# Kernel tuning notes

Measured on AMD Instinct MI355X. Metric: run time of the kernel, lower is better.

## Reference

```python
import jax, jax.numpy as jnp
import numpy as np

B, S, D, H = 2, 2048, 1024, 16
DH = D // H
EPS = 1e-5
NEG = -1e9


def _layer_norm(x, g, b):
    m = jnp.mean(x, axis=-1, keepdims=True)
    v = jnp.mean(jnp.square(x - m), axis=-1, keepdims=True)
    return (x - m) * jax.lax.rsqrt(v + EPS) * g + b


def setup_inputs() -> dict:
    key = jax.random.key(0)
    ks = jax.random.split(key, 10)
    std = 0.02
    inp = {
        "x": jax.random.normal(ks[0], (B, S, D), dtype=jnp.float32),
        "src_mask": jax.random.randint(ks[1], (B, S), 0, 2) > 0,
        # projection weights stored as (in, out) so y = x @ w + b
        "wq": jax.random.normal(ks[2], (D, D), dtype=jnp.float32) * std,
        "bq": jnp.zeros((D,), jnp.float32),
        "wk": jax.random.normal(ks[3], (D, D), dtype=jnp.float32) * std,
        "bk": jnp.zeros((D,), jnp.float32),
        "wv": jax.random.normal(ks[4], (D, D), dtype=jnp.float32) * std,
        "bv": jnp.zeros((D,), jnp.float32),
        "wo": jax.random.normal(ks[5], (D, D), dtype=jnp.float32) * std,
        "bo": jnp.zeros((D,), jnp.float32),
        "ln1_g": jnp.ones((D,), jnp.float32),
        "ln1_b": jnp.zeros((D,), jnp.float32),
        "w1": jax.random.normal(ks[6], (D, 2 * D), dtype=jnp.float32) * std,
        "b1": jnp.zeros((2 * D,), jnp.float32),
        "w2": jax.random.normal(ks[7], (2 * D, D), dtype=jnp.float32) * std,
        "b2": jnp.zeros((D,), jnp.float32),
        "ln2_g": jnp.ones((D,), jnp.float32),
        "ln2_b": jnp.zeros((D,), jnp.float32),
    }
    return inp


def reference(x, src_mask, wq, bq, wk, bk, wv, bv, wo, bo,
              ln1_g, ln1_b, w1, b1, w2, b2, ln2_g, ln2_b):
    b, s, d = x.shape
    # Q/K/V projections, split into heads: [B, S, H, DH]
    q = (x @ wq + bq).reshape(b, s, H, DH)
    k = (x @ wk + bk).reshape(b, s, H, DH)
    v = (x @ wv + bv).reshape(b, s, H, DH)
    # scaled scores [B, H, Sq, Sk] (matches torch's split/cat over heads)
    scores = jnp.einsum('bqhd,bkhd->bhqk', q, k) / jnp.sqrt(jnp.float32(DH))
    # additive key mask: -1e9 where src_mask is False
    scores = scores + jnp.where(src_mask, 0.0, NEG)[:, None, None, :]
    A = jax.nn.softmax(scores, axis=-1)
    attn = jnp.einsum('bhqk,bkhd->bqhd', A, v).reshape(b, s, d)
    attn_out = attn @ wo + bo + x
    h = _layer_norm(attn_out, ln1_g, ln1_b)
    ffn = jax.nn.relu(h @ w1 + b1) @ w2 + b2
    return _layer_norm(ffn + h, ln2_g, ln2_b)
```

## Files before the change

kernel.cpp:

```cpp
#include <hip/hip_runtime.h>
#include <math.h>

#define BB  2
#define SS  2048
#define DD  1024
#define HH  16
#define DHH 64
#define MM  (BB * SS)

typedef float f32x4 __attribute__((ext_vector_type(4)));
typedef short s16x8 __attribute__((ext_vector_type(8)));

__device__ __forceinline__ unsigned short f2b(float f) {
    union { float f; unsigned u; } v; v.f = f;
    unsigned r = v.u + 0x7fffu + ((v.u >> 16) & 1u);
    return (unsigned short)(r >> 16);
}
__device__ __forceinline__ float b2f(unsigned short u) {
    union { unsigned u; float f; } v; v.u = ((unsigned)u) << 16;
    return v.f;
}
__device__ __forceinline__ unsigned cvtpk(float lo, float hi) {
    unsigned r;
    asm("v_cvt_pk_bf16_f32 %0, %1, %2" : "=v"(r) : "v"(lo), "v"(hi));
    return r;
}

typedef __attribute__((address_space(1))) void gv_t;
typedef __attribute__((address_space(3))) void lv_t;
__device__ __forceinline__ void gld16(const void* g, void* l) {
    __builtin_amdgcn_global_load_lds((gv_t*)(void*)g, (lv_t*)l, 16, 0, 0);
}

__device__ __forceinline__ int sidx(int row, int col) {
    return row * 64 + (col ^ (((row + (row >> 3)) & 7) << 3));
}

template <int RELU, int RES, int OUTF, int VS>
__global__ __launch_bounds__(256)
void mgemm(const unsigned short* __restrict__ A, const unsigned short* __restrict__ B,
           const float* __restrict__ bias, const void* __restrict__ res,
           void* __restrict__ out, unsigned short* __restrict__ vt,
           int M, int N, int K, int outN)
{
    __shared__ short As[128 * 64];
    __shared__ short Bs[128 * 64];

    const int tid  = threadIdx.x;
    const int wave = tid >> 6, lane = tid & 63;
    const int bm = blockIdx.y * 128, bn = blockIdx.x * 128;
    const int srow = tid >> 3;
    const int scol = (tid & 7) * 8;
    const int wr = wave >> 1, wc = wave & 1;
    const int fr = lane & 15;
    const int fk = (lane >> 4) * 8;

    f32x4 acc[4][4];
#pragma unroll
    for (int i = 0; i < 4; ++i)
#pragma unroll
        for (int j = 0; j < 4; ++j) acc[i][j] = (f32x4){0.f, 0.f, 0.f, 0.f};

    for (int k0 = 0; k0 < K; k0 += 64) {
#pragma unroll
        for (int it = 0; it < 4; ++it) {
            gld16(&A[(size_t)(bm + it * 32 + srow) * K + k0 + scol],
                  &As[it * 2048 + wave * 512]);
            gld16(&B[(size_t)(bn + it * 32 + srow) * K + k0 + scol],
                  &Bs[it * 2048 + wave * 512]);
        }
        __syncthreads();

#pragma unroll
        for (int kk = 0; kk < 2; ++kk) {
            s16x8 af[4], bf[4];
#pragma unroll
            for (int i = 0; i < 4; ++i)
                af[i] = *(const s16x8*)&As[(wr * 64 + i * 16 + fr) * 64 + kk * 32 + fk];
#pragma unroll
            for (int j = 0; j < 4; ++j)
                bf[j] = *(const s16x8*)&Bs[(wc * 64 + j * 16 + fr) * 64 + kk * 32 + fk];
#pragma unroll
            for (int i = 0; i < 4; ++i)
#pragma unroll
                for (int j = 0; j < 4; ++j)
                    acc[i][j] = __builtin_amdgcn_mfma_f32_16x16x32_bf16(
                        af[i], bf[j], acc[i][j], 0, 0, 0);
        }
        __syncthreads();
    }

    const int r0 = bm + wr * 64 + (lane >> 4) * 4;
    const int c0 = bn + wc * 64 + (lane & 15);
    const float* resf          = (const float*)res;
    const unsigned short* resh = (const unsigned short*)res;
    float* outf          = (float*)out;
    unsigned short* outh = (unsigned short*)out;

    if (VS == 1 && bn >= 2048) {
#pragma unroll
        for (int i = 0; i < 4; ++i)
#pragma unroll
            for (int j = 0; j < 4; ++j) {
                const int col = c0 + j * 16;
                const int hh = (col >> 6) & 15, dh = col & 63;
                const float bcol = bias[col];
#pragma unroll
                for (int r = 0; r < 4; ++r) {
                    const int row = r0 + i * 16 + r;
                    const int bb = row >> 11, s = row & 2047;
                    vt[(size_t)(((bb * 16 + hh) * 64) + dh) * 2048 + s] =
                        f2b(acc[i][j][r] + bcol);
                }
            }
        return;
    }

#pragma unroll
    for (int i = 0; i < 4; ++i)
#pragma unroll
        for (int j = 0; j < 4; ++j) {
            const int col = c0 + j * 16;
            const float bcol = bias[col];
#pragma unroll
            for (int r = 0; r < 4; ++r) {
                const int row = r0 + i * 16 + r;
                float v = acc[i][j][r] + bcol;
                if (RES == 1) v += resf[(size_t)row * outN + col];
                if (RES == 2) v += b2f(resh[(size_t)row * outN + col]);
                if (RELU)     v = fmaxf(v, 0.f);
                if (OUTF) outf[(size_t)row * outN + col] = v;
                else      outh[(size_t)row * outN + col] = f2b(v);
            }
        }
}

__global__ __launch_bounds__(256)
void prep(const float* __restrict__ x,
          const float* __restrict__ wq, const float* __restrict__ wk,
          const float* __restrict__ wv, const float* __restrict__ wo,
          const float* __restrict__ w1, const float* __restrict__ w2,
          const float* __restrict__ bq, const float* __restrict__ bk,
          const float* __restrict__ bv,
          unsigned short* __restrict__ xb, unsigned short* __restrict__ wqkvT,
          unsigned short* __restrict__ woT, unsigned short* __restrict__ w1T,
          unsigned short* __restrict__ w2T, float* __restrict__ bqkv)
{
    __shared__ float T[64][65];
    const int tid = threadIdx.x;
    int bid = blockIdx.x;

    if (bid < 4096) {
        const int i = bid * 256 + tid;
        const float4 v = ((const float4*)x)[i];
        ushort4 o4;
        o4.x = f2b(v.x); o4.y = f2b(v.y); o4.z = f2b(v.z); o4.w = f2b(v.w);
        ((ushort4*)xb)[i] = o4;
        return;
    }
    bid -= 4096;

    if (bid >= 2048) {
        const int i = (bid - 2048) * 256 + tid;
        if (i < 1024) bqkv[i] = bq[i];
        else if (i < 2048) bqkv[i] = bk[i - 1024];
        else if (i < 3072) bqkv[i] = bv[i - 2048];
        return;
    }

    const float* src; unsigned short* dst; int K, N, nbx, sub;
    if (bid < 256)       { src = wq; dst = wqkvT;               K = 1024; N = 1024; nbx = 16; sub = bid; }
    else if (bid < 512)  { src = wk; dst = wqkvT + 1024 * 1024; K = 1024; N = 1024; nbx = 16; sub = bid - 256; }
    else if (bid < 768)  { src = wv; dst = wqkvT + 2048 * 1024; K = 1024; N = 1024; nbx = 16; sub = bid - 512; }
    else if (bid < 1024) { src = wo; dst = woT;                 K = 1024; N = 1024; nbx = 16; sub = bid - 768; }
    else if (bid < 1536) { src = w1; dst = w1T;                 K = 1024; N = 2048; nbx = 32; sub = bid - 1024; }
    else                 { src = w2; dst = w2T;                 K = 2048; N = 1024; nbx = 16; sub = bid - 1536; }

    const int n0 = (sub % nbx) * 64, k0 = (sub / nbx) * 64;
    const int c = tid & 63, rb = tid >> 6;
#pragma unroll
    for (int it = 0; it < 16; ++it) {
        const int r = it * 4 + rb;
        T[r][c] = src[(size_t)(k0 + r) * N + n0 + c];
    }
    __syncthreads();
#pragma unroll
    for (int it = 0; it < 16; ++it) {
        const int r = it * 4 + rb;
        dst[(size_t)(n0 + r) * K + k0 + c] = f2b(T[c][r]);
    }
}

__global__ __launch_bounds__(512)
void attn_mfma(const unsigned short* __restrict__ qk,
               const unsigned short* __restrict__ vt,
               const int* __restrict__ mask, unsigned short* __restrict__ o)
{
    const int b = blockIdx.z, h = blockIdx.y, q0 = blockIdx.x * 128;
    __shared__ unsigned short QP[8192];
    __shared__ unsigned short Ks[4096];
    __shared__ unsigned short Vs[4096];
    __shared__ float maskf[64];
    const int tid = threadIdx.x, wave = tid >> 6, lane = tid & 63;
    const int grp = lane >> 4, l16 = lane & 15;

    const size_t qkbase = (size_t)(b * SS) * 2048 + h * DHH;
    const size_t vbase  = (size_t)((b * HH + h) * 64) * 2048;
    const float SC = 0.18033688f;
    const float MNEG = -1.442695e9f;

#pragma unroll
    for (int it = 0; it < 2; ++it) {
        const int slot = it * 512 + tid;
        const int row = slot >> 3, dhb = slot & 7;
        const int src = (dhb ^ ((row + (row >> 3)) & 7)) * 8;
        gld16(&qk[qkbase + (size_t)(q0 + row) * 2048 + src],
              &QP[it * 4096 + wave * 512]);
    }
    const int krow = tid >> 3, kdhb = tid & 7;
    const int ksrc = (kdhb ^ ((krow + (krow >> 3)) & 7)) * 8;
    __syncthreads();
    const int prow = wave * 16 + l16;
    const s16x8 aq0 = *(const s16x8*)&QP[sidx(prow, grp * 8)];
    const s16x8 aq1 = *(const s16x8*)&QP[sidx(prow, 32 + grp * 8)];

    const s16x8 ones = {(short)0x3F80, (short)0x3F80, (short)0x3F80, (short)0x3F80,
                        (short)0x3F80, (short)0x3F80, (short)0x3F80, (short)0x3F80};

    f32x4 accO[4];
#pragma unroll
    for (int j = 0; j < 4; ++j) accO[j] = (f32x4){0.f, 0.f, 0.f, 0.f};
    f32x4 accS = (f32x4){0.f, 0.f, 0.f, 0.f};
    float mrow = -1e30f;

    for (int kt = 0; kt < SS / 64; ++kt) {
        const int kv0 = kt * 64;
        __syncthreads();
        gld16(&qk[qkbase + (size_t)(kv0 + krow) * 2048 + 1024 + ksrc], &Ks[wave * 512]);
        gld16(&vt[vbase + (size_t)krow * 2048 + kv0 + ksrc],           &Vs[wave * 512]);
        if (tid < 64) maskf[tid] = mask[b * SS + kv0 + tid] ? 0.f : MNEG;
        __syncthreads();

        f32x4 sv[4];
        __builtin_amdgcn_s_setprio(1);
#pragma unroll
        for (int j = 0; j < 4; ++j) {
            const s16x8 bk0 = *(const s16x8*)&Ks[sidx(j * 16 + l16, grp * 8)];
            const s16x8 bk1 = *(const s16x8*)&Ks[sidx(j * 16 + l16, 32 + grp * 8)];
            f32x4 z = (f32x4){0.f, 0.f, 0.f, 0.f};
            z = __builtin_amdgcn_mfma_f32_16x16x32_bf16(bk0, aq0, z, 0, 0, 0);
            z = __builtin_amdgcn_mfma_f32_16x16x32_bf16(bk1, aq1, z, 0, 0, 0);
            sv[j] = z;
        }
        __builtin_amdgcn_s_setprio(0);
#pragma unroll
        for (int j = 0; j < 4; ++j) {
            const float4 mv = *(const float4*)&maskf[j * 16 + grp * 4];
            sv[j][0] = sv[j][0] * SC + mv.x;
            sv[j][1] = sv[j][1] * SC + mv.y;
            sv[j][2] = sv[j][2] * SC + mv.z;
            sv[j][3] = sv[j][3] * SC + mv.w;
        }

        float mx = -1e30f;
#pragma unroll
        for (int j = 0; j < 4; ++j)
#pragma unroll
            for (int r = 0; r < 4; ++r) mx = fmaxf(mx, sv[j][r]);
        mx = fmaxf(mx, __shfl_xor(mx, 16));
        mx = fmaxf(mx, __shfl_xor(mx, 32));

        if (!__all(mx <= mrow + 8.f)) {
            const float mnew = fmaxf(mrow, mx);
            const float corrq = __builtin_amdgcn_exp2f(mrow - mnew);
            mrow = mnew;
            float cr[4];
#pragma unroll
            for (int r = 0; r < 4; ++r) cr[r] = __shfl(corrq, grp * 4 + r);
#pragma unroll
            for (int r = 0; r < 4; ++r) {
                accS[r] *= cr[r];
#pragma unroll
                for (int j = 0; j < 4; ++j) accO[j][r] *= cr[r];
            }
        }

#pragma unroll
        for (int j = 0; j < 4; ++j) {
            const float p0 = __builtin_amdgcn_exp2f(sv[j][0] - mrow);
            const float p1 = __builtin_amdgcn_exp2f(sv[j][1] - mrow);
            const float p2 = __builtin_amdgcn_exp2f(sv[j][2] - mrow);
            const float p3 = __builtin_amdgcn_exp2f(sv[j][3] - mrow);
            *(unsigned*)&QP[sidx(prow, j * 16 + grp * 4)]     = cvtpk(p0, p1);
            *(unsigned*)&QP[sidx(prow, j * 16 + grp * 4 + 2)] = cvtpk(p2, p3);
        }

        const s16x8 pa0 = *(const s16x8*)&QP[sidx(prow, grp * 8)];
        const s16x8 pa1 = *(const s16x8*)&QP[sidx(prow, 32 + grp * 8)];
        __builtin_amdgcn_s_setprio(1);
        accS = __builtin_amdgcn_mfma_f32_16x16x32_bf16(pa0, ones, accS, 0, 0, 0);
        accS = __builtin_amdgcn_mfma_f32_16x16x32_bf16(pa1, ones, accS, 0, 0, 0);
#pragma unroll
        for (int j = 0; j < 4; ++j) {
            const s16x8 vb0 = *(const s16x8*)&Vs[sidx(j * 16 + l16, grp * 8)];
            const s16x8 vb1 = *(const s16x8*)&Vs[sidx(j * 16 + l16, 32 + grp * 8)];
            accO[j] = __builtin_amdgcn_mfma_f32_16x16x32_bf16(pa0, vb0, accO[j], 0, 0, 0);
            accO[j] = __builtin_amdgcn_mfma_f32_16x16x32_bf16(pa1, vb1, accO[j], 0, 0, 0);
        }
        __builtin_amdgcn_s_setprio(0);
    }

#pragma unroll
    for (int r = 0; r < 4; ++r) {
        const float inv = 1.0f / accS[r];
        const int row = q0 + wave * 16 + grp * 4 + r;
#pragma unroll
        for (int j = 0; j < 4; ++j)
            o[(size_t)(b * SS + row) * DD + h * DHH + j * 16 + l16] =
                f2b(accO[j][r] * inv);
    }
}

template <int OUTBF>
__global__ __launch_bounds__(256)
void ln_kernel(const float* __restrict__ x, const float* __restrict__ g,
               const float* __restrict__ beta, void* __restrict__ outv)
{
    const int row = blockIdx.x;
    const int tid = threadIdx.x;
    const float4 xl = reinterpret_cast<const float4*>(x + (size_t)row * DD)[tid];
    float s  = xl.x + xl.y + xl.z + xl.w;
    float sq = xl.x * xl.x + xl.y * xl.y + xl.z * xl.z + xl.w * xl.w;
#pragma unroll
    for (int off = 1; off < 64; off <<= 1) {
        s  += __shfl_xor(s, off);
        sq += __shfl_xor(sq, off);
    }
    __shared__ float ssum[4], ssq[4];
    const int wid = tid >> 6;
    if ((tid & 63) == 0) { ssum[wid] = s; ssq[wid] = sq; }
    __syncthreads();
    s  = ssum[0] + ssum[1] + ssum[2] + ssum[3];
    sq = ssq[0]  + ssq[1]  + ssq[2]  + ssq[3];
    const float mean = s * (1.0f / DD);
    const float var  = fmaxf(sq * (1.0f / DD) - mean * mean, 0.0f);
    const float rstd = rsqrtf(var + 1e-5f);
    const float4 gv = reinterpret_cast<const float4*>(g)[tid];
    const float4 bv = reinterpret_cast<const float4*>(beta)[tid];
    float4 ov;
    ov.x = (xl.x - mean) * rstd * gv.x + bv.x;
    ov.y = (xl.y - mean) * rstd * gv.y + bv.y;
    ov.z = (xl.z - mean) * rstd * gv.z + bv.z;
    ov.w = (xl.w - mean) * rstd * gv.w + bv.w;
    if (OUTBF) {
        ushort4 o4;
        o4.x = f2b(ov.x); o4.y = f2b(ov.y); o4.z = f2b(ov.z); o4.w = f2b(ov.w);
        reinterpret_cast<ushort4*>(outv)[(size_t)row * 256 + tid] = o4;
    } else {
        reinterpret_cast<float4*>(outv)[(size_t)row * 256 + tid] = ov;
    }
}

extern "C" void kernel_launch(void* const* d_in, const int* in_sizes, int n_in,
                              void* d_out, int out_size, void* d_ws, size_t ws_size,
                              hipStream_t stream)
{
    (void)in_sizes; (void)n_in; (void)out_size; (void)ws_size;

    const float* x     = (const float*)d_in[0];
    const int*   mask  = (const int*)  d_in[1];
    const float* wq    = (const float*)d_in[2];
    const float* bq    = (const float*)d_in[3];
    const float* wk    = (const float*)d_in[4];
    const float* bk    = (const float*)d_in[5];
    const float* wv    = (const float*)d_in[6];
    const float* bv    = (const float*)d_in[7];
    const float* wo    = (const float*)d_in[8];
    const float* bo    = (const float*)d_in[9];
    const float* ln1_g = (const float*)d_in[10];
    const float* ln1_b = (const float*)d_in[11];
    const float* w1    = (const float*)d_in[12];
    const float* b1    = (const float*)d_in[13];
    const float* w2    = (const float*)d_in[14];
    const float* b2    = (const float*)d_in[15];
    const float* ln2_g = (const float*)d_in[16];
    const float* ln2_b = (const float*)d_in[17];

    float* out = (float*)d_out;
    char*  wsb = (char*)d_ws;
    const size_t MB = 1u << 20;

    unsigned short* wqkvT = (unsigned short*)(wsb + 0);
    unsigned short* woT   = (unsigned short*)(wsb + 6 * MB);
    unsigned short* w1T   = (unsigned short*)(wsb + 8 * MB);
    unsigned short* w2T   = (unsigned short*)(wsb + 12 * MB);
    float*          bqkv  = (float*)(wsb + 16 * MB);
    unsigned short* qkb   = (unsigned short*)(wsb + 17 * MB);
    unsigned short* vtb   = (unsigned short*)(wsb + 33 * MB);
    unsigned short* xb    = (unsigned short*)(wsb + 41 * MB);
    unsigned short* ab16  = xb;
    float*          t0    = (float*)(wsb + 17 * MB);
    unsigned short* hb16  = (unsigned short*)(wsb + 33 * MB);
    unsigned short* f1b   = (unsigned short*)(wsb + 41 * MB);
    float*          t1    = (float*)(wsb + 17 * MB);

    prep<<<6156, 256, 0, stream>>>(x, wq, wk, wv, wo, w1, w2, bq, bk, bv,
                                   xb, wqkvT, woT, w1T, w2T, bqkv);
    mgemm<0, 0, 0, 1><<<dim3(24, 32), 256, 0, stream>>>(
        xb, wqkvT, bqkv, nullptr, qkb, vtb, MM, 3 * DD, DD, 2048);
    attn_mfma<<<dim3(SS / 128, HH, BB), 512, 0, stream>>>(qkb, vtb, mask, ab16);
    mgemm<0, 1, 1, 0><<<dim3(8, 32), 256, 0, stream>>>(
        ab16, woT, bo, x, t0, nullptr, MM, DD, DD, DD);
    ln_kernel<1><<<MM, 256, 0, stream>>>(t0, ln1_g, ln1_b, hb16);
    mgemm<1, 0, 0, 0><<<dim3(16, 32), 256, 0, stream>>>(
        hb16, w1T, b1, nullptr, f1b, nullptr, MM, 2 * DD, DD, 2 * DD);
    mgemm<0, 2, 1, 0><<<dim3(8, 32), 256, 0, stream>>>(
        f1b, w2T, b2, hb16, t1, nullptr, MM, DD, 2 * DD, DD);
    ln_kernel<0><<<MM, 256, 0, stream>>>(t1, ln2_g, ln2_b, out);
}
```

Baseline: 242.7 us.

## Double-buffer GEMM LDS tiles, swizzle block order, shrink attention blocks

The GEMM kernel now keeps two LDS buffers so the async global-to-LDS load of the next K tile is issued before computing the current one, with one barrier per iteration instead of two. Workgroup IDs are remapped in an XCD-style swizzle so that neighbouring tiles run together and share cache. Attention blocks drop from 128 queries and 8 waves to 64 queries and 4 waves, giving twice as many blocks with less LDS each, and each thread now loads two K/V chunks. These changes target exposed load latency, cache locality and occupancy, at the cost of more LDS in the GEMM (64KB) and more K/V reloads across attention blocks.

```diff
diff --git a/kernel.cpp b/kernel.cpp
--- a/kernel.cpp
+++ b/kernel.cpp
@@ -43,12 +43,19 @@
            void* __restrict__ out, unsigned short* __restrict__ vt,
            int M, int N, int K, int outN)
 {
-    __shared__ short As[128 * 64];
-    __shared__ short Bs[128 * 64];
+    __shared__ short As[2][128 * 64];
+    __shared__ short Bs[2][128 * 64];
 
     const int tid  = threadIdx.x;
     const int wave = tid >> 6, lane = tid & 63;
-    const int bm = blockIdx.y * 128, bn = blockIdx.x * 128;
+
+    const int nwg = gridDim.x * gridDim.y;
+    const int bid = blockIdx.y * gridDim.x + blockIdx.x;
+    const int swz = (bid & 7) * (nwg >> 3) + (bid >> 3);
+    const int by = swz / gridDim.x;
+    const int bx = swz - by * gridDim.x;
+    const int bm = by * 128, bn = bx * 128;
+
     const int srow = tid >> 3;
     const int scol = (tid & 7) * 8;
     const int wr = wave >> 1, wc = wave & 1;
@@ -61,25 +68,25 @@
 #pragma unroll
         for (int j = 0; j < 4; ++j) acc[i][j] = (f32x4){0.f, 0.f, 0.f, 0.f};
 
-    for (int k0 = 0; k0 < K; k0 += 64) {
+    auto stage = [&](int buf, int k0) {
 #pragma unroll
         for (int it = 0; it < 4; ++it) {
             gld16(&A[(size_t)(bm + it * 32 + srow) * K + k0 + scol],
-                  &As[it * 2048 + wave * 512]);
+                  &As[buf][it * 2048 + wave * 512]);
             gld16(&B[(size_t)(bn + it * 32 + srow) * K + k0 + scol],
-                  &Bs[it * 2048 + wave * 512]);
-        }
-        __syncthreads();
-
+                  &Bs[buf][it * 2048 + wave * 512]);
+        }
+    };
+    auto compute = [&](int buf) {
 #pragma unroll
         for (int kk = 0; kk < 2; ++kk) {
             s16x8 af[4], bf[4];
 #pragma unroll
             for (int i = 0; i < 4; ++i)
-                af[i] = *(const s16x8*)&As[(wr * 64 + i * 16 + fr) * 64 + kk * 32 + fk];
+                af[i] = *(const s16x8*)&As[buf][(wr * 64 + i * 16 + fr) * 64 + kk * 32 + fk];
 #pragma unroll
             for (int j = 0; j < 4; ++j)
-                bf[j] = *(const s16x8*)&Bs[(wc * 64 + j * 16 + fr) * 64 + kk * 32 + fk];
+                bf[j] = *(const s16x8*)&Bs[buf][(wc * 64 + j * 16 + fr) * 64 + kk * 32 + fk];
 #pragma unroll
             for (int i = 0; i < 4; ++i)
 #pragma unroll
@@ -87,8 +94,19 @@
                     acc[i][j] = __builtin_amdgcn_mfma_f32_16x16x32_bf16(
                         af[i], bf[j], acc[i][j], 0, 0, 0);
         }
+    };
+
+    const int nk = K >> 6;
+    stage(0, 0);
+    __syncthreads();
+    int cur = 0;
+    for (int t = 0; t < nk - 1; ++t) {
+        stage(cur ^ 1, (t + 1) << 6);
+        compute(cur);
         __syncthreads();
-    }
+        cur ^= 1;
+    }
+    compute(cur);
 
     const int r0 = bm + wr * 64 + (lane >> 4) * 4;
     const int c0 = bn + wc * 64 + (lane & 15);
@@ -191,13 +209,13 @@
     }
 }
 
-__global__ __launch_bounds__(512)
+__global__ __launch_bounds__(256)
 void attn_mfma(const unsigned short* __restrict__ qk,
                const unsigned short* __restrict__ vt,
                const int* __restrict__ mask, unsigned short* __restrict__ o)
 {
-    const int b = blockIdx.z, h = blockIdx.y, q0 = blockIdx.x * 128;
-    __shared__ unsigned short QP[8192];
+    const int b = blockIdx.z, h = blockIdx.y, q0 = blockIdx.x * 64;
+    __shared__ unsigned short QP[4096];
     __shared__ unsigned short Ks[4096];
     __shared__ unsigned short Vs[4096];
     __shared__ float maskf[64];
@@ -209,16 +227,15 @@
     const float SC = 0.18033688f;
     const float MNEG = -1.442695e9f;
 
+    const int row0 = tid >> 3, dhb = tid & 7;
+
 #pragma unroll
     for (int it = 0; it < 2; ++it) {
-        const int slot = it * 512 + tid;
-        const int row = slot >> 3, dhb = slot & 7;
+        const int row = it * 32 + row0;
         const int src = (dhb ^ ((row + (row >> 3)) & 7)) * 8;
         gld16(&qk[qkbase + (size_t)(q0 + row) * 2048 + src],
-              &QP[it * 4096 + wave * 512]);
-    }
-    const int krow = tid >> 3, kdhb = tid & 7;
-    const int ksrc = (kdhb ^ ((krow + (krow >> 3)) & 7)) * 8;
+              &QP[(it * 256 + wave * 64) * 8]);
+    }
     __syncthreads();
     const int prow = wave * 16 + l16;
     const s16x8 aq0 = *(const s16x8*)&QP[sidx(prow, grp * 8)];
@@ -236,8 +253,15 @@
     for (int kt = 0; kt < SS / 64; ++kt) {
         const int kv0 = kt * 64;
         __syncthreads();
-        gld16(&qk[qkbase + (size_t)(kv0 + krow) * 2048 + 1024 + ksrc], &Ks[wave * 512]);
-        gld16(&vt[vbase + (size_t)krow * 2048 + kv0 + ksrc],           &Vs[wave * 512]);
+#pragma unroll
+        for (int it = 0; it < 2; ++it) {
+            const int row = it * 32 + row0;
+            const int src = (dhb ^ ((row + (row >> 3)) & 7)) * 8;
+            gld16(&qk[qkbase + (size_t)(kv0 + row) * 2048 + 1024 + src],
+                  &Ks[(it * 256 + wave * 64) * 8]);
+            gld16(&vt[vbase + (size_t)row * 2048 + kv0 + src],
+                  &Vs[(it * 256 + wave * 64) * 8]);
+        }
         if (tid < 64) maskf[tid] = mask[b * SS + kv0 + tid] ? 0.f : MNEG;
         __syncthreads();
 
@@ -408,7 +432,7 @@
                                    xb, wqkvT, woT, w1T, w2T, bqkv);
     mgemm<0, 0, 0, 1><<<dim3(24, 32), 256, 0, stream>>>(
         xb, wqkvT, bqkv, nullptr, qkb, vtb, MM, 3 * DD, DD, 2048);
-    attn_mfma<<<dim3(SS / 128, HH, BB), 512, 0, stream>>>(qkb, vtb, mask, ab16);
+    attn_mfma<<<dim3(SS / 64, HH, BB), 256, 0, stream>>>(qkb, vtb, mask, ab16);
     mgemm<0, 1, 1, 0><<<dim3(8, 32), 256, 0, stream>>>(
         ab16, woT, bo, x, t0, nullptr, MM, DD, DD, DD);
     ln_kernel<1><<<MM, 256, 0, stream>>>(t0, ln1_g, ln1_b, hb16);
```

After: 299.7 us. 1.24x slower.
